# Optimization experiments

Measured on AMD Instinct MI355X. Metric: run time of the kernel, lower is better.

Reference implementation:

```python
import jax, jax.numpy as jnp
import numpy as np

WS = 16            # window height = width
DIM = 512          # channels
H = 16             # num heads
HD = DIM // H      # head dim = 32
NW = 64            # num windows per image (mask leading dim)
B_ = 256           # num_windows * batch
N_IN = 512         # pre-stride sequence length
SCALE = HD ** -0.5
MAX_SEQ = 512
STRIDE = 2


def _relative_position_index(wh, ww):
    coords = np.stack(np.meshgrid(np.arange(wh), np.arange(ww), indexing='ij'))  # (2, wh, ww)
    cf = coords.reshape(2, -1)                             # (2, wh*ww)
    rc = (cf[:, :, None] - cf[:, None, :]).transpose(1, 2, 0).astype(np.int32)
    rc[:, :, 0] += wh - 1
    rc[:, :, 1] += ww - 1
    rc[:, :, 0] *= 2 * ww - 1
    return rc.sum(-1)                                      # (wh*ww, wh*ww)


def setup_inputs() -> dict:
    key = jax.random.key(0)
    ks = jax.random.split(key, 8)
    x = jax.random.normal(ks[0], (B_, N_IN, DIM), dtype=jnp.float32)
    y = jax.random.normal(ks[1], (B_, N_IN, DIM), dtype=jnp.float32)
    mask = jax.random.normal(ks[2], (NW, WS * WS, WS * WS), dtype=jnp.float32)
    q_w = jax.random.normal(ks[3], (DIM, DIM), dtype=jnp.float32) * 0.02
    q_b = jnp.zeros((DIM,), dtype=jnp.float32)
    kv_w = jax.random.normal(ks[4], (2 * DIM, DIM), dtype=jnp.float32) * 0.02
    kv_b = jnp.zeros((2 * DIM,), dtype=jnp.float32)
    proj_w = jax.random.normal(ks[5], (DIM, DIM), dtype=jnp.float32) * 0.02
    proj_b = jnp.zeros((DIM,), dtype=jnp.float32)
    bias_table = jax.random.normal(ks[6], ((2 * WS - 1) ** 2, H), dtype=jnp.float32) * 0.02
    rel_pos_index = jnp.asarray(_relative_position_index(WS, WS))  # (256, 256) int32
    return {"x": x, "y": y, "mask": mask, "q_w": q_w, "q_b": q_b,
            "kv_w": kv_w, "kv_b": kv_b, "proj_w": proj_w, "proj_b": proj_b,
            "bias_table": bias_table, "rel_pos_index": rel_pos_index}


def reference(x, y, mask, q_w, q_b, kv_w, kv_b, proj_w, proj_b, bias_table, rel_pos_index):
    # truncate + stride (as in forward)
    x = x[:, :MAX_SEQ][:, ::STRIDE]          # (B_, N, C), N = 256
    y = y[:, :MAX_SEQ][:, ::STRIDE]
    b, n, c = x.shape
    # projections
    q = (x @ q_w.T + q_b).reshape(b, n, H, HD).transpose(0, 2, 1, 3)   # (B_, H, N, D)
    kv = y @ kv_w.T + kv_b                                              # (B_, N, 2C)
    k = kv[..., :DIM].reshape(b, n, H, HD).transpose(0, 2, 1, 3)
    v = kv[..., DIM:].reshape(b, n, H, HD).transpose(0, 2, 1, 3)
    # scores
    attn = jnp.einsum('bhnd,bhmd->bhnm', q * SCALE, k)                  # (B_, H, N, N)
    # gathered relative position bias: (N, N, H) -> (H, N, N)
    rpb = bias_table[rel_pos_index].transpose(2, 0, 1)
    attn = attn + rpb[None]
    # window mask: view (B_//nW, nW, H, N, N) + mask[None,:,None]
    attn = attn.reshape(b // NW, NW, H, n, n) + mask[None, :, None]
    attn = attn.reshape(b, H, n, n)
    attn = jax.nn.softmax(attn, axis=-1)
    out = jnp.einsum('bhnm,bhmd->bhnd', attn, v)                        # (B_, H, N, D)
    out = out.transpose(0, 2, 1, 3).reshape(b, n, DIM)
    out = out @ proj_w.T + proj_b
    return out
```

## Files before the change

### kernel.cpp

```cpp
#include <hip/hip_runtime.h>

typedef _Float16 half8 __attribute__((ext_vector_type(8)));
typedef _Float16 half4 __attribute__((ext_vector_type(4)));
typedef _Float16 half2v __attribute__((ext_vector_type(2)));
typedef float f32x4 __attribute__((ext_vector_type(4)));

#define LOG2E 1.4426950408889634f
#define QSCALE (0.17677669529663687f * 1.4426950408889634f)

static __device__ __forceinline__ half4 cvt4h(float4 v) {
    half2v a = __builtin_bit_cast(half2v, __builtin_amdgcn_cvt_pkrtz(v.x, v.y));
    half2v b = __builtin_bit_cast(half2v, __builtin_amdgcn_cvt_pkrtz(v.z, v.w));
    return half4{ a[0], a[1], b[0], b[1] };
}

__global__ __launch_bounds__(256) void prep_kernel(
    const float* __restrict__ mask, const float* __restrict__ table,
    const int* __restrict__ rpi, _Float16* __restrict__ maskh,
    _Float16* __restrict__ rpbh)
{
    int i = blockIdx.x * 256 + threadIdx.x;
    float4 v = ((const float4*)mask)[i];
    half4 hv = { (_Float16)(v.x * LOG2E), (_Float16)(v.y * LOG2E),
                 (_Float16)(v.z * LOG2E), (_Float16)(v.w * LOG2E) };
    *(half4*)(maskh + (size_t)i * 4) = hv;
    int p = i & 65535, hh = i >> 16;
    rpbh[i] = (_Float16)(table[rpi[p] * 16 + hh] * LOG2E);
}

__global__ __launch_bounds__(256) void proj_qkv(
    const float* __restrict__ inp, const float* __restrict__ wgt,
    const float* __restrict__ bias, _Float16* __restrict__ qout,
    _Float16* __restrict__ kout, _Float16* __restrict__ vout, int which)
{
    __shared__ __align__(16) _Float16 As[128 * 64];
    __shared__ __align__(16) _Float16 Ws[128 * 64];
    const int nwg = gridDim.x;
    const int chunk = nwg >> 3;
    const int f = blockIdx.x;
    const int swz = (f & 7) * chunk + (f >> 3);
    const int nct_sh = (which == 0) ? 2 : 3;
    const int ct = swz & ((1 << nct_sh) - 1);
    const int rt = swz >> nct_sh;

    const int t = threadIdx.x;
    const int lane = t & 63, wave = t >> 6;
    const int ql = lane & 15, g = lane >> 4;
    const int wr = (wave >> 1) * 64, wc = (wave & 1) * 64;

    f32x4 acc[4][4] = {};

    const int srr = t >> 4;
    const int sc4 = (t & 15) * 4;
    for (int kk = 0; kk < 8; ++kk) {
        const int k0 = kk * 64;
#pragma unroll
        for (int p = 0; p < 8; ++p) {
            int rr = p * 16 + srr;
            int r = rt * 128 + rr;
            size_t irow = ((size_t)(r >> 8) * 512 + (size_t)((r & 255) * 2)) * 512;
            float4 av = *(const float4*)(inp + irow + k0 + sc4);
            int boff = rr * 128 + ((sc4 * 2) ^ ((rr & 7) << 4));
            *(half4*)((char*)As + boff) = cvt4h(av);
            int wrow = ct * 128 + rr;
            float4 wv = *(const float4*)(wgt + (size_t)wrow * 512 + k0 + sc4);
            *(half4*)((char*)Ws + boff) = cvt4h(wv);
        }
        __syncthreads();
#pragma unroll
        for (int kh = 0; kh < 2; ++kh) {
            half8 af[4], bf[4];
#pragma unroll
            for (int i = 0; i < 4; ++i) {
                int row = wr + i * 16 + ql;
                af[i] = *(const half8*)((const char*)As + row * 128 +
                        ((kh * 64 + g * 16) ^ ((ql & 7) << 4)));
            }
#pragma unroll
            for (int j = 0; j < 4; ++j) {
                int row = wc + j * 16 + ql;
                bf[j] = *(const half8*)((const char*)Ws + row * 128 +
                        ((kh * 64 + g * 16) ^ ((ql & 7) << 4)));
            }
#pragma unroll
            for (int i = 0; i < 4; ++i)
#pragma unroll
                for (int j = 0; j < 4; ++j)
                    acc[i][j] = __builtin_amdgcn_mfma_f32_16x16x32_f16(af[i], bf[j], acc[i][j], 0, 0, 0);
        }
        __syncthreads();
    }

    const float scale = (which == 0) ? QSCALE : 1.0f;
#pragma unroll
    for (int j = 0; j < 4; ++j) {
        int c = ct * 128 + wc + j * 16 + ql;
        float bv = bias[c];
#pragma unroll
        for (int i = 0; i < 4; ++i) {
#pragma unroll
            for (int rr = 0; rr < 4; ++rr) {
                int r = rt * 128 + wr + i * 16 + g * 4 + rr;
                float val = (acc[i][j][rr] + bv) * scale;
                _Float16 hv = (_Float16)val;
                int b = r >> 8, n = r & 255;
                if (which == 0) {
                    int hh = c >> 5, d = c & 31;
                    qout[((size_t)(b * 16 + hh) * 256 + n) * 32 + d] = hv;
                } else if (c < 512) {
                    int hh = c >> 5, d = c & 31;
                    kout[((size_t)(b * 16 + hh) * 256 + n) * 32 + d] = hv;
                } else {
                    int c2 = c - 512, hh = c2 >> 5, d = c2 & 31;
                    vout[((size_t)(b * 16 + hh) * 256 + n) * 32 + d] = hv;
                }
            }
        }
    }
}

__global__ __launch_bounds__(256, 2) void attn_kernel(
    const _Float16* __restrict__ Q, const _Float16* __restrict__ K,
    const _Float16* __restrict__ V, const _Float16* __restrict__ rpbh,
    const _Float16* __restrict__ maskh, _Float16* __restrict__ pre)
{
    __shared__ __align__(16) _Float16 bias_s[2][16 * 256];
    const int blk = blockIdx.x;
    const int w = blk >> 4, h = blk & 15;
    const int t = threadIdx.x;
    const int lane = t & 63, wave = t >> 6;
    const int ql = lane & 15, g = lane >> 4;
    const int b = w + 64 * wave;
    const size_t blk_b = (size_t)(b * 16 + h) * 8192;
    const _Float16* Qp = Q + blk_b + g * 8;
    const _Float16* Kp = K + blk_b + ql * 32 + g * 8;
    const _Float16* rp = rpbh + (size_t)h * 65536;
    const _Float16* mp = maskh + (size_t)w * 65536;

    half8 karr[16];
#pragma unroll
    for (int tt = 0; tt < 16; ++tt)
        karr[tt] = *(const half8*)(Kp + tt * 512);

    half4 vf0[16], vf1[16];
    {
        const _Float16* vb = V + blk_b + g * 128 + ql;
#pragma unroll
        for (int tt = 0; tt < 16; ++tt) {
#pragma unroll
            for (int j = 0; j < 4; ++j) {
                vf0[tt][j] = vb[tt * 512 + j * 32];
                vf1[tt][j] = vb[tt * 512 + j * 32 + 16];
            }
        }
    }

    const int sq = t >> 4;
    const int scb = (t & 15) * 32;
    const int sw = sq << 3;
    const int sgoff = (t & 15) * 16;

    {
        const _Float16* rrow = rp + (size_t)sq * 256 + sgoff;
        const _Float16* mrow = mp + (size_t)sq * 256 + sgoff;
        half8 s0 = *(const half8*)rrow + *(const half8*)mrow;
        half8 s1 = *(const half8*)(rrow + 8) + *(const half8*)(mrow + 8);
        char* sb = (char*)bias_s[0] + sq * 512;
        *(half4*)(sb + ((scb) ^ sw))      = __builtin_shufflevector(s0, s0, 0, 1, 2, 3);
        *(half4*)(sb + ((scb + 8) ^ sw))  = __builtin_shufflevector(s0, s0, 4, 5, 6, 7);
        *(half4*)(sb + ((scb + 16) ^ sw)) = __builtin_shufflevector(s1, s1, 0, 1, 2, 3);
        *(half4*)(sb + ((scb + 24) ^ sw)) = __builtin_shufflevector(s1, s1, 4, 5, 6, 7);
    }
    __syncthreads();

#pragma unroll 1
    for (int qg = 0; qg < 16; ++qg) {
        const int q0 = qg * 16;
        half8 nr0, nm0, nr1, nm1;
        if (qg < 15) {
            const _Float16* rrow = rp + (size_t)(q0 + 16 + sq) * 256 + sgoff;
            const _Float16* mrow = mp + (size_t)(q0 + 16 + sq) * 256 + sgoff;
            nr0 = *(const half8*)rrow;
            nm0 = *(const half8*)mrow;
            nr1 = *(const half8*)(rrow + 8);
            nm1 = *(const half8*)(mrow + 8);
        }

        const int q = q0 + ql;
        half8 qf = *(const half8*)(Qp + (size_t)q * 32);
        const char* bb = (const char*)bias_s[qg & 1] + ql * 512;
        f32x4 lsum = { 0.f, 0.f, 0.f, 0.f };
        f32x4 o0 = { 0.f, 0.f, 0.f, 0.f }, o1 = { 0.f, 0.f, 0.f, 0.f };
#pragma unroll
        for (int tt = 0; tt < 16; ++tt) {
            half4 bs = *(const half4*)(bb + ((tt * 32 + g * 8) ^ (ql << 3)));
            f32x4 bf = { (float)bs[0], (float)bs[1], (float)bs[2], (float)bs[3] };
            f32x4 s = __builtin_amdgcn_mfma_f32_16x16x32_f16(karr[tt], qf, bf, 0, 0, 0);
            float e0 = __builtin_amdgcn_exp2f(s[0]);
            float e1 = __builtin_amdgcn_exp2f(s[1]);
            float e2 = __builtin_amdgcn_exp2f(s[2]);
            float e3 = __builtin_amdgcn_exp2f(s[3]);
            lsum[0] += e0; lsum[1] += e1; lsum[2] += e2; lsum[3] += e3;
            half2v p01 = __builtin_bit_cast(half2v, __builtin_amdgcn_cvt_pkrtz(e0, e1));
            half2v p23 = __builtin_bit_cast(half2v, __builtin_amdgcn_cvt_pkrtz(e2, e3));
            half4 pf = { p01[0], p01[1], p23[0], p23[1] };
            o0 = __builtin_amdgcn_mfma_f32_16x16x16f16(pf, vf0[tt], o0, 0, 0, 0);
            o1 = __builtin_amdgcn_mfma_f32_16x16x16f16(pf, vf1[tt], o1, 0, 0, 0);
        }
        float l = (lsum[0] + lsum[1]) + (lsum[2] + lsum[3]);
        l += __shfl_xor(l, 16);
        l += __shfl_xor(l, 32);
#pragma unroll
        for (int rr = 0; rr < 4; ++rr) {
            float inv = __builtin_amdgcn_rcpf(__shfl(l, g * 4 + rr));
            int row = q0 + g * 4 + rr;
            size_t ob = ((size_t)b * 256 + row) * 512 + h * 32;
            pre[ob + ql] = (_Float16)(o0[rr] * inv);
            pre[ob + 16 + ql] = (_Float16)(o1[rr] * inv);
        }
        if (qg < 15) {
            half8 s0 = nr0 + nm0, s1 = nr1 + nm1;
            char* sb = (char*)bias_s[(qg + 1) & 1] + sq * 512;
            *(half4*)(sb + ((scb) ^ sw))      = __builtin_shufflevector(s0, s0, 0, 1, 2, 3);
            *(half4*)(sb + ((scb + 8) ^ sw))  = __builtin_shufflevector(s0, s0, 4, 5, 6, 7);
            *(half4*)(sb + ((scb + 16) ^ sw)) = __builtin_shufflevector(s1, s1, 0, 1, 2, 3);
            *(half4*)(sb + ((scb + 24) ^ sw)) = __builtin_shufflevector(s1, s1, 4, 5, 6, 7);
        }
        __syncthreads();
    }
}

__global__ __launch_bounds__(256) void proj_out_kernel(
    const _Float16* __restrict__ pre, const float* __restrict__ wgt,
    const float* __restrict__ bias, float* __restrict__ out)
{
    __shared__ __align__(16) _Float16 As[128 * 64];
    __shared__ __align__(16) _Float16 Ws[128 * 64];
    const int nwg = gridDim.x;
    const int chunk = nwg >> 3;
    const int f = blockIdx.x;
    const int swz = (f & 7) * chunk + (f >> 3);
    const int ct = swz & 3;
    const int rt = swz >> 2;

    const int t = threadIdx.x;
    const int lane = t & 63, wave = t >> 6;
    const int ql = lane & 15, g = lane >> 4;
    const int wr = (wave >> 1) * 64, wc = (wave & 1) * 64;

    f32x4 acc[4][4] = {};
    const int srr = t >> 4, sc4 = (t & 15) * 4;
    const int arr = t >> 3, ac8 = (t & 7) * 8;
    for (int kk = 0; kk < 8; ++kk) {
        const int k0 = kk * 64;
#pragma unroll
        for (int p = 0; p < 4; ++p) {
            int rr = p * 32 + arr;
            half8 v = *(const half8*)(pre + (size_t)(rt * 128 + rr) * 512 + k0 + ac8);
            *(half8*)((char*)As + rr * 128 + ((ac8 * 2) ^ ((rr & 7) << 4))) = v;
        }
#pragma unroll
        for (int p = 0; p < 8; ++p) {
            int rr = p * 16 + srr;
            float4 wv = *(const float4*)(wgt + (size_t)(ct * 128 + rr) * 512 + k0 + sc4);
            *(half4*)((char*)Ws + rr * 128 + ((sc4 * 2) ^ ((rr & 7) << 4))) = cvt4h(wv);
        }
        __syncthreads();
#pragma unroll
        for (int kh = 0; kh < 2; ++kh) {
            half8 af[4], bf[4];
#pragma unroll
            for (int i = 0; i < 4; ++i) {
                int row = wr + i * 16 + ql;
                af[i] = *(const half8*)((const char*)As + row * 128 +
                        ((kh * 64 + g * 16) ^ ((ql & 7) << 4)));
            }
#pragma unroll
            for (int j = 0; j < 4; ++j) {
                int row = wc + j * 16 + ql;
                bf[j] = *(const half8*)((const char*)Ws + row * 128 +
                        ((kh * 64 + g * 16) ^ ((ql & 7) << 4)));
            }
#pragma unroll
            for (int i = 0; i < 4; ++i)
#pragma unroll
                for (int j = 0; j < 4; ++j)
                    acc[i][j] = __builtin_amdgcn_mfma_f32_16x16x32_f16(af[i], bf[j], acc[i][j], 0, 0, 0);
        }
        __syncthreads();
    }
#pragma unroll
    for (int j = 0; j < 4; ++j) {
        int c = ct * 128 + wc + j * 16 + ql;
        float bv = bias[c];
#pragma unroll
        for (int i = 0; i < 4; ++i)
#pragma unroll
            for (int rr = 0; rr < 4; ++rr) {
                int r = rt * 128 + wr + i * 16 + g * 4 + rr;
                out[(size_t)r * 512 + c] = acc[i][j][rr] + bv;
            }
    }
}

extern "C" void kernel_launch(void* const* d_in, const int* in_sizes, int n_in,
                              void* d_out, int out_size, void* d_ws, size_t ws_size,
                              hipStream_t stream)
{
    const float* x      = (const float*)d_in[0];
    const float* y      = (const float*)d_in[1];
    const float* mask   = (const float*)d_in[2];
    const float* q_w    = (const float*)d_in[3];
    const float* q_b    = (const float*)d_in[4];
    const float* kv_w   = (const float*)d_in[5];
    const float* kv_b   = (const float*)d_in[6];
    const float* proj_w = (const float*)d_in[7];
    const float* proj_b = (const float*)d_in[8];
    const float* btab   = (const float*)d_in[9];
    const int*   rpi    = (const int*)d_in[10];
    float* out = (float*)d_out;

    char* ws = (char*)d_ws;
    _Float16* Qw  = (_Float16*)(ws);
    _Float16* Kw  = (_Float16*)(ws + ((size_t)64 << 20));
    _Float16* Vw  = (_Float16*)(ws + ((size_t)128 << 20));
    _Float16* Pre = (_Float16*)(ws + ((size_t)192 << 20));
    _Float16* Rpb = (_Float16*)(ws + ((size_t)256 << 20));
    _Float16* Mh  = (_Float16*)(ws + ((size_t)256 << 20) + 2097152);

    prep_kernel<<<4096, 256, 0, stream>>>(mask, btab, rpi, Mh, Rpb);
    proj_qkv<<<2048, 256, 0, stream>>>(x, q_w, q_b, Qw, Kw, Vw, 0);
    proj_qkv<<<4096, 256, 0, stream>>>(y, kv_w, kv_b, Qw, Kw, Vw, 1);
    attn_kernel<<<1024, 256, 0, stream>>>(Qw, Kw, Vw, Rpb, Mh, Pre);
    proj_out_kernel<<<2048, 256, 0, stream>>>(Pre, proj_w, proj_b, out);
}
```

Measured before the change: 510.1 us.

## Pre-convert inputs and weights to fp16 and unify GEMMs into one kernel

Adds a single convert kernel that strides and converts x and y to fp16, and converts all three weight matrices to fp16 once, folding the Q scale into the weights. It also merges mask and bias prep into that launch. The three projection GEMMs share one fp16 kernel that loads half8 tiles and issues global loads before the barrier to overlap them. This removes repeated fp32 weight loads and per-tile conversion in every GEMM block, at the cost of an extra read-write pass over the strided inputs and workspace buffer reuse (K stored over X, pre-projection over Y).

```diff
diff --git a/kernel.cpp b/kernel.cpp
--- a/kernel.cpp
+++ b/kernel.cpp
@@ -14,24 +14,65 @@
     return half4{ a[0], a[1], b[0], b[1] };
 }
 
-__global__ __launch_bounds__(256) void prep_kernel(
-    const float* __restrict__ mask, const float* __restrict__ table,
-    const int* __restrict__ rpi, _Float16* __restrict__ maskh,
+#define NB_X 16384
+#define NB_Y 16384
+#define NB_W 512
+#define NB_M 4096
+#define NB_R 4096
+
+__global__ __launch_bounds__(256) void convert_kernel(
+    const float* __restrict__ x, const float* __restrict__ y,
+    const float* __restrict__ q_w, const float* __restrict__ kv_w,
+    const float* __restrict__ proj_w, const float* __restrict__ mask,
+    const float* __restrict__ table, const int* __restrict__ rpi,
+    _Float16* __restrict__ Xh, _Float16* __restrict__ Yh,
+    _Float16* __restrict__ Wh, _Float16* __restrict__ maskh,
     _Float16* __restrict__ rpbh)
 {
-    int i = blockIdx.x * 256 + threadIdx.x;
-    float4 v = ((const float4*)mask)[i];
-    half4 hv = { (_Float16)(v.x * LOG2E), (_Float16)(v.y * LOG2E),
-                 (_Float16)(v.z * LOG2E), (_Float16)(v.w * LOG2E) };
-    *(half4*)(maskh + (size_t)i * 4) = hv;
-    int p = i & 65535, hh = i >> 16;
-    rpbh[i] = (_Float16)(table[rpi[p] * 16 + hh] * LOG2E);
-}
-
-__global__ __launch_bounds__(256) void proj_qkv(
-    const float* __restrict__ inp, const float* __restrict__ wgt,
-    const float* __restrict__ bias, _Float16* __restrict__ qout,
-    _Float16* __restrict__ kout, _Float16* __restrict__ vout, int which)
+    const int blk = blockIdx.x, t = threadIdx.x;
+    if (blk < NB_X + NB_Y) {
+        const float* src; _Float16* dst; int v;
+        if (blk < NB_X) { v = blk * 256 + t; src = x; dst = Xh; }
+        else { v = (blk - NB_X) * 256 + t; src = y; dst = Yh; }
+        int r = v >> 6, ks = (v & 63) * 8;
+        const float* s = src + ((size_t)(r >> 8) * 512 + (size_t)((r & 255) * 2)) * 512 + ks;
+        half4 h0 = cvt4h(*(const float4*)s);
+        half4 h1 = cvt4h(*(const float4*)(s + 4));
+        half8 hv = { h0[0], h0[1], h0[2], h0[3], h1[0], h1[1], h1[2], h1[3] };
+        *(half8*)(dst + (size_t)v * 8) = hv;
+    } else if (blk < NB_X + NB_Y + NB_W) {
+        int v = (blk - NB_X - NB_Y) * 256 + t;
+        int row = v >> 6, ks = (v & 63) * 8;
+        const float* s; float sc = 1.0f;
+        if (row < 512)       { s = q_w + (size_t)row * 512;            sc = QSCALE; }
+        else if (row < 1536) { s = kv_w + (size_t)(row - 512) * 512; }
+        else                 { s = proj_w + (size_t)(row - 1536) * 512; }
+        float4 a = *(const float4*)(s + ks);
+        float4 b = *(const float4*)(s + ks + 4);
+        a.x *= sc; a.y *= sc; a.z *= sc; a.w *= sc;
+        b.x *= sc; b.y *= sc; b.z *= sc; b.w *= sc;
+        half4 h0 = cvt4h(a), h1 = cvt4h(b);
+        half8 hv = { h0[0], h0[1], h0[2], h0[3], h1[0], h1[1], h1[2], h1[3] };
+        *(half8*)(Wh + (size_t)v * 8) = hv;
+    } else if (blk < NB_X + NB_Y + NB_W + NB_M) {
+        int i = (blk - NB_X - NB_Y - NB_W) * 256 + t;
+        float4 v = ((const float4*)mask)[i];
+        half4 hv = { (_Float16)(v.x * LOG2E), (_Float16)(v.y * LOG2E),
+                     (_Float16)(v.z * LOG2E), (_Float16)(v.w * LOG2E) };
+        *(half4*)(maskh + (size_t)i * 4) = hv;
+    } else {
+        int i = (blk - NB_X - NB_Y - NB_W - NB_M) * 256 + t;
+        int p = i & 65535, hh = i >> 16;
+        rpbh[i] = (_Float16)(table[rpi[p] * 16 + hh] * LOG2E);
+    }
+}
+
+__global__ __launch_bounds__(256) void gemm_f16(
+    const _Float16* __restrict__ Ah, const _Float16* __restrict__ Wh,
+    const float* __restrict__ bias, float bscale,
+    _Float16* __restrict__ qout, _Float16* __restrict__ kout,
+    _Float16* __restrict__ vout, float* __restrict__ fout,
+    int mode, int nct_sh)
 {
     __shared__ __align__(16) _Float16 As[128 * 64];
     __shared__ __align__(16) _Float16 Ws[128 * 64];
@@ -39,7 +80,6 @@
     const int chunk = nwg >> 3;
     const int f = blockIdx.x;
     const int swz = (f & 7) * chunk + (f >> 3);
-    const int nct_sh = (which == 0) ? 2 : 3;
     const int ct = swz & ((1 << nct_sh) - 1);
     const int rt = swz >> nct_sh;
 
@@ -48,24 +88,33 @@
     const int ql = lane & 15, g = lane >> 4;
     const int wr = (wave >> 1) * 64, wc = (wave & 1) * 64;
 
+    const int sr = t >> 3;
+    const int st = t & 7;
+    const _Float16* aR = Ah + ((size_t)(rt * 128 + sr)) * 512 + st * 8;
+    const _Float16* wR = Wh + ((size_t)(ct * 128 + sr)) * 512 + st * 8;
+    char* asw = (char*)As + sr * 128 + ((st ^ (sr & 7)) << 4);
+    char* wsw = (char*)Ws + sr * 128 + ((st ^ (sr & 7)) << 4);
+
     f32x4 acc[4][4] = {};
-
-    const int srr = t >> 4;
-    const int sc4 = (t & 15) * 4;
     for (int kk = 0; kk < 8; ++kk) {
         const int k0 = kk * 64;
-#pragma unroll
-        for (int p = 0; p < 8; ++p) {
-            int rr = p * 16 + srr;
-            int r = rt * 128 + rr;
-            size_t irow = ((size_t)(r >> 8) * 512 + (size_t)((r & 255) * 2)) * 512;
-            float4 av = *(const float4*)(inp + irow + k0 + sc4);
-            int boff = rr * 128 + ((sc4 * 2) ^ ((rr & 7) << 4));
-            *(half4*)((char*)As + boff) = cvt4h(av);
-            int wrow = ct * 128 + rr;
-            float4 wv = *(const float4*)(wgt + (size_t)wrow * 512 + k0 + sc4);
-            *(half4*)((char*)Ws + boff) = cvt4h(wv);
-        }
+        half8 a0 = *(const half8*)(aR + k0);
+        half8 a1 = *(const half8*)(aR + 32 * 512 + k0);
+        half8 a2 = *(const half8*)(aR + 64 * 512 + k0);
+        half8 a3 = *(const half8*)(aR + 96 * 512 + k0);
+        half8 w0 = *(const half8*)(wR + k0);
+        half8 w1 = *(const half8*)(wR + 32 * 512 + k0);
+        half8 w2 = *(const half8*)(wR + 64 * 512 + k0);
+        half8 w3 = *(const half8*)(wR + 96 * 512 + k0);
+        if (kk) __syncthreads();
+        *(half8*)(asw)           = a0;
+        *(half8*)(asw + 32*128)  = a1;
+        *(half8*)(asw + 64*128)  = a2;
+        *(half8*)(asw + 96*128)  = a3;
+        *(half8*)(wsw)           = w0;
+        *(half8*)(wsw + 32*128)  = w1;
+        *(half8*)(wsw + 64*128)  = w2;
+        *(half8*)(wsw + 96*128)  = w3;
         __syncthreads();
 #pragma unroll
         for (int kh = 0; kh < 2; ++kh) {
@@ -74,13 +123,13 @@
             for (int i = 0; i < 4; ++i) {
                 int row = wr + i * 16 + ql;
                 af[i] = *(const half8*)((const char*)As + row * 128 +
-                        ((kh * 64 + g * 16) ^ ((ql & 7) << 4)));
+                        (((kh * 4 + g) ^ (ql & 7)) << 4));
             }
 #pragma unroll
             for (int j = 0; j < 4; ++j) {
                 int row = wc + j * 16 + ql;
                 bf[j] = *(const half8*)((const char*)Ws + row * 128 +
-                        ((kh * 64 + g * 16) ^ ((ql & 7) << 4)));
+                        (((kh * 4 + g) ^ (ql & 7)) << 4));
             }
 #pragma unroll
             for (int i = 0; i < 4; ++i)
@@ -88,31 +137,33 @@
                 for (int j = 0; j < 4; ++j)
                     acc[i][j] = __builtin_amdgcn_mfma_f32_16x16x32_f16(af[i], bf[j], acc[i][j], 0, 0, 0);
         }
-        __syncthreads();
-    }
-
-    const float scale = (which == 0) ? QSCALE : 1.0f;
+    }
+
 #pragma unroll
     for (int j = 0; j < 4; ++j) {
         int c = ct * 128 + wc + j * 16 + ql;
-        float bv = bias[c];
+        float bv = bias[c] * bscale;
 #pragma unroll
         for (int i = 0; i < 4; ++i) {
 #pragma unroll
             for (int rr = 0; rr < 4; ++rr) {
                 int r = rt * 128 + wr + i * 16 + g * 4 + rr;
-                float val = (acc[i][j][rr] + bv) * scale;
-                _Float16 hv = (_Float16)val;
-                int b = r >> 8, n = r & 255;
-                if (which == 0) {
-                    int hh = c >> 5, d = c & 31;
-                    qout[((size_t)(b * 16 + hh) * 256 + n) * 32 + d] = hv;
-                } else if (c < 512) {
-                    int hh = c >> 5, d = c & 31;
-                    kout[((size_t)(b * 16 + hh) * 256 + n) * 32 + d] = hv;
+                float val = acc[i][j][rr] + bv;
+                if (mode == 2) {
+                    fout[(size_t)r * 512 + c] = val;
                 } else {
-                    int c2 = c - 512, hh = c2 >> 5, d = c2 & 31;
-                    vout[((size_t)(b * 16 + hh) * 256 + n) * 32 + d] = hv;
+                    _Float16 hv = (_Float16)val;
+                    int b = r >> 8, n = r & 255;
+                    if (mode == 0) {
+                        int hh = c >> 5, d = c & 31;
+                        qout[((size_t)(b * 16 + hh) * 256 + n) * 32 + d] = hv;
+                    } else if (c < 512) {
+                        int hh = c >> 5, d = c & 31;
+                        kout[((size_t)(b * 16 + hh) * 256 + n) * 32 + d] = hv;
+                    } else {
+                        int c2 = c - 512, hh = c2 >> 5, d = c2 & 31;
+                        vout[((size_t)(b * 16 + hh) * 256 + n) * 32 + d] = hv;
+                    }
                 }
             }
         }
@@ -230,79 +281,6 @@
     }
 }
 
-__global__ __launch_bounds__(256) void proj_out_kernel(
-    const _Float16* __restrict__ pre, const float* __restrict__ wgt,
-    const float* __restrict__ bias, float* __restrict__ out)
-{
-    __shared__ __align__(16) _Float16 As[128 * 64];
-    __shared__ __align__(16) _Float16 Ws[128 * 64];
-    const int nwg = gridDim.x;
-    const int chunk = nwg >> 3;
-    const int f = blockIdx.x;
-    const int swz = (f & 7) * chunk + (f >> 3);
-    const int ct = swz & 3;
-    const int rt = swz >> 2;
-
-    const int t = threadIdx.x;
-    const int lane = t & 63, wave = t >> 6;
-    const int ql = lane & 15, g = lane >> 4;
-    const int wr = (wave >> 1) * 64, wc = (wave & 1) * 64;
-
-    f32x4 acc[4][4] = {};
-    const int srr = t >> 4, sc4 = (t & 15) * 4;
-    const int arr = t >> 3, ac8 = (t & 7) * 8;
-    for (int kk = 0; kk < 8; ++kk) {
-        const int k0 = kk * 64;
-#pragma unroll
-        for (int p = 0; p < 4; ++p) {
-            int rr = p * 32 + arr;
-            half8 v = *(const half8*)(pre + (size_t)(rt * 128 + rr) * 512 + k0 + ac8);
-            *(half8*)((char*)As + rr * 128 + ((ac8 * 2) ^ ((rr & 7) << 4))) = v;
-        }
-#pragma unroll
-        for (int p = 0; p < 8; ++p) {
-            int rr = p * 16 + srr;
-            float4 wv = *(const float4*)(wgt + (size_t)(ct * 128 + rr) * 512 + k0 + sc4);
-            *(half4*)((char*)Ws + rr * 128 + ((sc4 * 2) ^ ((rr & 7) << 4))) = cvt4h(wv);
-        }
-        __syncthreads();
-#pragma unroll
-        for (int kh = 0; kh < 2; ++kh) {
-            half8 af[4], bf[4];
-#pragma unroll
-            for (int i = 0; i < 4; ++i) {
-                int row = wr + i * 16 + ql;
-                af[i] = *(const half8*)((const char*)As + row * 128 +
-                        ((kh * 64 + g * 16) ^ ((ql & 7) << 4)));
-            }
-#pragma unroll
-            for (int j = 0; j < 4; ++j) {
-                int row = wc + j * 16 + ql;
-                bf[j] = *(const half8*)((const char*)Ws + row * 128 +
-                        ((kh * 64 + g * 16) ^ ((ql & 7) << 4)));
-            }
-#pragma unroll
-            for (int i = 0; i < 4; ++i)
-#pragma unroll
-                for (int j = 0; j < 4; ++j)
-                    acc[i][j] = __builtin_amdgcn_mfma_f32_16x16x32_f16(af[i], bf[j], acc[i][j], 0, 0, 0);
-        }
-        __syncthreads();
-    }
-#pragma unroll
-    for (int j = 0; j < 4; ++j) {
-        int c = ct * 128 + wc + j * 16 + ql;
-        float bv = bias[c];
-#pragma unroll
-        for (int i = 0; i < 4; ++i)
-#pragma unroll
-            for (int rr = 0; rr < 4; ++rr) {
-                int r = rt * 128 + wr + i * 16 + g * 4 + rr;
-                out[(size_t)r * 512 + c] = acc[i][j][rr] + bv;
-            }
-    }
-}
-
 extern "C" void kernel_launch(void* const* d_in, const int* in_sizes, int n_in,
                               void* d_out, int out_size, void* d_ws, size_t ws_size,
                               hipStream_t stream)
@@ -321,16 +299,21 @@
     float* out = (float*)d_out;
 
     char* ws = (char*)d_ws;
-    _Float16* Qw  = (_Float16*)(ws);
-    _Float16* Kw  = (_Float16*)(ws + ((size_t)64 << 20));
-    _Float16* Vw  = (_Float16*)(ws + ((size_t)128 << 20));
-    _Float16* Pre = (_Float16*)(ws + ((size_t)192 << 20));
-    _Float16* Rpb = (_Float16*)(ws + ((size_t)256 << 20));
-    _Float16* Mh  = (_Float16*)(ws + ((size_t)256 << 20) + 2097152);
-
-    prep_kernel<<<4096, 256, 0, stream>>>(mask, btab, rpi, Mh, Rpb);
-    proj_qkv<<<2048, 256, 0, stream>>>(x, q_w, q_b, Qw, Kw, Vw, 0);
-    proj_qkv<<<4096, 256, 0, stream>>>(y, kv_w, kv_b, Qw, Kw, Vw, 1);
-    attn_kernel<<<1024, 256, 0, stream>>>(Qw, Kw, Vw, Rpb, Mh, Pre);
-    proj_out_kernel<<<2048, 256, 0, stream>>>(Pre, proj_w, proj_b, out);
-}
+    _Float16* XK  = (_Float16*)(ws);
+    _Float16* YP  = (_Float16*)(ws + ((size_t)64 << 20));
+    _Float16* Qw  = (_Float16*)(ws + ((size_t)128 << 20));
+    _Float16* Vw  = (_Float16*)(ws + ((size_t)192 << 20));
+    _Float16* Wh  = (_Float16*)(ws + ((size_t)256 << 20));
+    _Float16* Rpb = (_Float16*)(ws + ((size_t)258 << 20));
+    _Float16* Mh  = (_Float16*)(ws + ((size_t)260 << 20));
+
+    convert_kernel<<<NB_X + NB_Y + NB_W + NB_M + NB_R, 256, 0, stream>>>(
+        x, y, q_w, kv_w, proj_w, mask, btab, rpi, XK, YP, Wh, Mh, Rpb);
+    gemm_f16<<<2048, 256, 0, stream>>>(XK, Wh, q_b, QSCALE,
+                                       Qw, nullptr, nullptr, nullptr, 0, 2);
+    gemm_f16<<<4096, 256, 0, stream>>>(YP, Wh + 512 * 512, kv_b, 1.0f,
+                                       nullptr, XK, Vw, nullptr, 1, 3);
+    attn_kernel<<<1024, 256, 0, stream>>>(Qw, XK, Vw, Rpb, Mh, YP);
+    gemm_f16<<<2048, 256, 0, stream>>>(YP, Wh + 1536 * 512, proj_b, 1.0f,
+                                       nullptr, nullptr, nullptr, out, 2, 2);
+}
```

Result: no change. 501.2 us (-1.8%).
